# Optimization experiments

Hardware: AMD Instinct MI355X
Metric: run time of the kernel (lower is better)

## Reference

```python
import jax, jax.numpy as jnp
import numpy as np

V = 16000   # src/trg vocab
E = 512     # embedding dim (encoder_dim = decoder_dim)
H = 512     # hidden_size
L = 2       # n_layers
S = 128     # src len
T = 128     # trg len
B = 64      # batch


def _lstm_stack(x, Wih, Whh, bih, bhh, h0, c0):
    """Multi-layer LSTM, PyTorch gate order (i, f, g, o).
    x: [T, B, E]; Wih/Whh: [L, 4H, *]; bih/bhh: [L, 4H]; h0/c0: [L, B, H].
    Returns (outputs [T,B,H], hN [L,B,H], cN [L,B,H]). Dropout is eval-mode (identity)."""
    inp = x
    hs, cs = [], []
    for l in range(Wih.shape[0]):
        W1, W2 = Wih[l], Whh[l]
        b = bih[l] + bhh[l]
        def step(carry, xt, W1=W1, W2=W2, b=b):
            h, c = carry
            g = xt @ W1.T + h @ W2.T + b          # [B, 4H]
            i, f, gg, o = jnp.split(g, 4, axis=-1)
            c = jax.nn.sigmoid(f) * c + jax.nn.sigmoid(i) * jnp.tanh(gg)
            h = jax.nn.sigmoid(o) * jnp.tanh(c)
            return (h, c), h
        (h, c), ys = jax.lax.scan(step, (h0[l], c0[l]), inp)
        inp = ys
        hs.append(h)
        cs.append(c)
    return inp, jnp.stack(hs), jnp.stack(cs)


def setup_inputs() -> dict:
    key = jax.random.key(0)
    ks = jax.random.split(key, 16)
    u = lambda k, shape: jax.random.uniform(k, shape, jnp.float32, -0.08, 0.08)
    inp = {
        "src": jax.random.randint(ks[0], (S, B), 0, V),
        "trg": jax.random.randint(ks[1], (T, B), 0, V),
        "teacher_forcing_ratio": 1,
        "enc_emb": u(ks[2], (V, E)),
        "dec_emb": u(ks[3], (V, E)),
        "enc_Wih": jnp.stack([u(ks[4], (4 * H, E)), u(ks[5], (4 * H, H))]),
        "enc_Whh": u(ks[6], (L, 4 * H, H)),
        "enc_bih": u(ks[7], (L, 4 * H)),
        "enc_bhh": u(ks[8], (L, 4 * H)),
        "dec_Wih": jnp.stack([u(ks[9], (4 * H, E)), u(ks[10], (4 * H, H))]),
        "dec_Whh": u(ks[11], (L, 4 * H, H)),
        "dec_bih": u(ks[12], (L, 4 * H)),
        "dec_bhh": u(ks[13], (L, 4 * H)),
        "out_W": u(ks[14], (V, H)),
        "out_b": u(ks[15], (V,)),
    }
    return inp


def reference(src, trg, teacher_forcing_ratio, enc_emb, dec_emb,
              enc_Wih, enc_Whh, enc_bih, enc_bhh,
              dec_Wih, dec_Whh, dec_bih, dec_bhh, out_W, out_b):
    # Encoder: embed + 2-layer LSTM over src; keep final (h, c).
    zeros = jnp.zeros((L, B, H), enc_emb.dtype)
    _, h, c = _lstm_stack(enc_emb[src], enc_Wih, enc_Whh, enc_bih, enc_bhh, zeros, zeros)
    # Decoder: teacher_forcing_ratio=1 => input at step t is trg[t-1];
    # the per-step python loop collapses to one LSTM scan over trg[:-1].
    dec_in = dec_emb[trg[:-1]]                    # [T-1, B, E]
    ys, _, _ = _lstm_stack(dec_in, dec_Wih, dec_Whh, dec_bih, dec_bhh, h, c)
    logits = jnp.einsum('tbh,vh->tbv', ys, out_W) + out_b   # [T-1, B, V]
    # original: outputs[1:].view(-1, V)
    return logits.reshape(-1, V)
```

## Files before the change

kernel.cpp:

```cpp
#include <hip/hip_runtime.h>


typedef __attribute__((ext_vector_type(8))) short v8s;
typedef __attribute__((ext_vector_type(4))) short v4s;
typedef __attribute__((ext_vector_type(8))) _Float16 v8h;
typedef __attribute__((ext_vector_type(4))) float v4f;
typedef __attribute__((ext_vector_type(4))) unsigned int v4u;

#define AS1 __attribute__((address_space(1)))
#define AS3 __attribute__((address_space(3)))

__device__ __forceinline__ short f2h(float x) {
  _Float16 h = (_Float16)x;
  return __builtin_bit_cast(short, h);
}
__device__ __forceinline__ void gload16(const void* g, void* l) {
  __builtin_amdgcn_global_load_lds((const AS1 void*)g, (AS3 void*)l, 16, 0, 0);
}
__device__ __forceinline__ float sigf(float x) { return 1.f / (1.f + __expf(-x)); }
__device__ __forceinline__ float tanhfast(float x) { return 2.f / (1.f + __expf(-2.f * x)) - 1.f; }

__device__ __forceinline__ void ld16_sc1(v4u& d, const void* p) {
  asm volatile("global_load_dwordx4 %0, %1, off sc1" : "=v"(d) : "v"(p) : "memory");
}
__device__ __forceinline__ void ld16(v4u& d, const void* p) {
  asm volatile("global_load_dwordx4 %0, %1, off" : "=v"(d) : "v"(p));
}

__device__ __forceinline__ void poll32(const unsigned* flags, int base, unsigned tgt) {
  int lane = threadIdx.x & 63;
  const unsigned* fp = flags + base + (lane & 31);
  while (true) {
    unsigned v;
    asm volatile("global_load_dword %0, %1, off sc1\n\ts_waitcnt vmcnt(0)"
                 : "=v"(v) : "v"(fp) : "memory");
    if (__all((int)((lane >= 32) || (v >= tgt)))) break;
    __builtin_amdgcn_s_sleep(1);
  }
}

struct ConvJobs {
  const float* src[8];
  short* dst[8];
  int coloff[8];
};
__global__ void conv8(ConvJobs J) {
  int j = blockIdx.y;
  int i = blockIdx.x * 256 + threadIdx.x;
  int r = i >> 7, k4 = (i & 127) * 4;
  int rr = ((r >> 4) & 31) * 64 + (r >> 9) * 16 + (r & 15);
  float4 v = *(const float4*)(J.src[j] + (size_t)r * 512 + k4);
  v4s s; s[0] = f2h(v.x); s[1] = f2h(v.y); s[2] = f2h(v.z); s[3] = f2h(v.w);
  *(v4s*)(J.dst[j] + (size_t)rr * 1024 + J.coloff[j] + k4) = s;
}

__global__ void conv_ow(const float* __restrict__ in, short* __restrict__ out) {
  int i = blockIdx.x * 256 + threadIdx.x;
  if (i >= 16000 * 128) return;
  int r = i >> 7, k4 = (i & 127) * 4;
  float4 v = *(const float4*)(in + (size_t)r * 512 + k4);
  v4s s; s[0] = f2h(v.x); s[1] = f2h(v.y); s[2] = f2h(v.z); s[3] = f2h(v.w);
  *(v4s*)(out + (size_t)r * 512 + k4) = s;
}

struct BiasJobs {
  const float* a[4];
  const float* b[4];
  float* o[4];
};
__global__ void conv_b4(BiasJobs J) {
  int j = blockIdx.y;
  int r = blockIdx.x * 256 + threadIdx.x;
  if (r < 2048)
    J.o[j][((r >> 4) & 31) * 64 + (r >> 9) * 16 + (r & 15)] = J.a[j][r] + J.b[j][r];
}

__global__ void zero3(short* a, short* b, short* c, unsigned* f) {
  int i = blockIdx.x * 256 + threadIdx.x;
  if (i < 32768) { a[i] = 0; b[i] = 0; c[i] = 0; }
  if (i < 64) f[i] = 0;
}

__global__ void embed_all(const int* __restrict__ src, const int* __restrict__ trg,
                          const float* __restrict__ ee, const float* __restrict__ de,
                          short* __restrict__ out) {
  int row = blockIdx.x;
  int e = threadIdx.x * 2;
  const float* emb;
  int id;
  if (row < 8192) { id = src[row]; emb = ee; }
  else { id = trg[row - 8192]; emb = de; }
  float2 v = *(const float2*)(emb + (size_t)id * 512 + e);
  unsigned pack = ((unsigned)(unsigned short)f2h(v.y) << 16) | (unsigned short)f2h(v.x);
  *(unsigned*)(out + (size_t)row * 512 + e) = pack;
}

#define GF_BIAS 2
#define GF_GUARDM 4

__global__ __launch_bounds__(256, 2) void gemm_bt(
    const short* __restrict__ Am, const short* __restrict__ Bm,
    const float* __restrict__ bias, float* __restrict__ Cm,
    int M, int N, int K, int ldc, int flags) {
  __shared__ __align__(16) char smem[65536];
  short* lA = (short*)smem;
  short* lB = (short*)(smem + 32768);
  const int tid = threadIdx.x, lane = tid & 63, wave = tid >> 6;
  const int wm = wave >> 1, wn = wave & 1;
  const int tm = blockIdx.y, tn = blockIdx.x;
  v4f acc[4][4] = {};
  const short* Abase = Am + (size_t)tm * 128 * K;
  const short* Bbase = Bm + (size_t)tn * 128 * K;

  for (int kt = 0; kt < K; kt += 128) {
    __syncthreads();
#pragma unroll
    for (int i2 = 0; i2 < 8; ++i2) {
      int c = (wave * 8 + i2) * 64 + lane;
      int row = c >> 4, ch = c & 15;
      int sch = ch ^ (row & 15);
      gload16(Abase + (size_t)row * K + kt + sch * 8, (char*)lA + c * 16);
      gload16(Bbase + (size_t)row * K + kt + sch * 8, (char*)lB + c * 16);
    }
    asm volatile("s_waitcnt vmcnt(0)" ::: "memory");
    __syncthreads();
#pragma unroll
    for (int kc = 0; kc < 4; ++kc) {
      v8h af[4], bh[4];
#pragma unroll
      for (int mt = 0; mt < 4; ++mt) {
        int row = wm * 64 + mt * 16 + (lane & 15);
        af[mt] = *(const v8h*)((const char*)lA + row * 256 +
                               ((kc * 64 + (lane >> 4) * 16) ^ ((row & 15) << 4)));
      }
#pragma unroll
      for (int nt = 0; nt < 4; ++nt) {
        int row = wn * 64 + nt * 16 + (lane & 15);
        bh[nt] = *(const v8h*)((const char*)lB + row * 256 +
                               ((kc * 64 + (lane >> 4) * 16) ^ ((row & 15) << 4)));
      }
#pragma unroll
      for (int mt = 0; mt < 4; ++mt)
#pragma unroll
        for (int nt = 0; nt < 4; ++nt)
          acc[mt][nt] = __builtin_amdgcn_mfma_f32_16x16x32_f16(af[mt], bh[nt], acc[mt][nt], 0, 0, 0);
    }
  }

  __syncthreads();
  float* ft = (float*)smem;
#pragma unroll
  for (int mt = 0; mt < 4; ++mt)
#pragma unroll
    for (int nt = 0; nt < 4; ++nt)
#pragma unroll
      for (int rg = 0; rg < 4; ++rg) {
        int r = wm * 64 + mt * 16 + (lane >> 4) * 4 + rg;
        int c = wn * 64 + nt * 16 + (lane & 15);
        ft[r * 128 + c] = acc[mt][nt][rg];
      }
  __syncthreads();
  const int c4 = (tid & 31) * 4;
  const int gcol = tn * 128 + c4;
  float4 bv = make_float4(0.f, 0.f, 0.f, 0.f);
  if (flags & GF_BIAS) bv = *(const float4*)(bias + gcol);
#pragma unroll
  for (int it = 0; it < 16; ++it) {
    int r = it * 8 + (tid >> 5);
    int gr = tm * 128 + r;
    if ((flags & GF_GUARDM) && gr >= M) continue;
    float4 v = *(const float4*)(ft + r * 128 + c4);
    v.x += bv.x; v.y += bv.y; v.z += bv.z; v.w += bv.w;
    *(float4*)(Cm + (size_t)gr * ldc + gcol) = v;
  }
}

struct PipeArgs {
  const short* W0e;
  const short* W0d;
  const short* W1e;
  const short* W1d;
  const short* X;
  const float* b0e;
  const float* b0d;
  const float* b1e;
  const float* b1d;
  short* h0;
  short* h1;
  unsigned* flags;
  int Tenc, Ttot;
};

#define SLOT 32768

__global__ __launch_bounds__(256, 1) void lstm_pipe(PipeArgs A) {
  __shared__ __align__(16) short Wlds[64 * 1024];
  __shared__ __align__(16) short hsm[64 * 16];
  const int tid = threadIdx.x, lane = tid & 63, wave = tid >> 6;
  const int w = blockIdx.x, layer = w >> 5, wl = w & 31;

  auto stage = [&](const short* Wsrc) {
    for (int i = tid * 8; i < 64 * 1024; i += 256 * 8) {
      int row = i >> 10, k = i & 1023;
      v8s v = *(const v8s*)(Wsrc + (size_t)row * 1024 + k);
      *(v8s*)((char*)Wlds + row * 2048 + ((k * 2) ^ ((row & 7) << 4))) = v;
    }
  };
  stage((layer ? A.W1e : A.W0e) + (size_t)(wl * 64) * 1024);

  const int uu = lane & 15;
  float beV[4], bdV[4];
#pragma unroll
  for (int g = 0; g < 4; ++g) {
    beV[g] = (layer ? A.b1e : A.b0e)[wl * 64 + g * 16 + uu];
    bdV[g] = (layer ? A.b1d : A.b0d)[wl * 64 + g * 16 + uu];
  }
  float creg[4] = {0.f, 0.f, 0.f, 0.f};

  const int arow = wave * 16 + uu;
  const int koff = (lane >> 4) * 8;
  const size_t aoff = (size_t)arow * 512 + koff;
  __syncthreads();

  for (int t = 0; t < A.Ttot; ++t) {
    if (t == A.Tenc) {
      stage((layer ? A.W1d : A.W0d) + (size_t)(wl * 64) * 1024);
      __syncthreads();
    }

    v4f acc[4] = {};

    if (layer) {
      if (wave == 0) poll32(A.flags, 0, (unsigned)(t + 1));
      __syncthreads();
    }
    {
      const short* p1 = (layer ? (A.h0 + (size_t)(t + 1) * SLOT)
                               : (A.X + (size_t)t * SLOT)) + aoff;
      v4u fa[16];
      if (layer) {
#pragma unroll
        for (int kc = 0; kc < 16; ++kc) ld16_sc1(fa[kc], p1 + kc * 32);
      } else {
#pragma unroll
        for (int kc = 0; kc < 16; ++kc) ld16(fa[kc], p1 + kc * 32);
      }
      asm volatile("s_waitcnt vmcnt(0)" ::: "memory");
      __builtin_amdgcn_sched_barrier(0);
#pragma unroll
      for (int kc = 0; kc < 16; ++kc) {
        v8h af = __builtin_bit_cast(v8h, fa[kc]);
        int kg = kc * 32 + koff;
#pragma unroll
        for (int nt = 0; nt < 4; ++nt) {
          int wrow = nt * 16 + uu;
          v8h bh = *(const v8h*)((const char*)Wlds + wrow * 2048 +
                                 ((kg * 2) ^ ((wrow & 7) << 4)));
          acc[nt] = __builtin_amdgcn_mfma_f32_16x16x32_f16(af, bh, acc[nt], 0, 0, 0);
        }
      }
    }

    if (t > 0) {
      if (wave == 0) poll32(A.flags, layer ? 32 : 0, (unsigned)t);
      __syncthreads();
    }
    {
      const short* p2 = ((layer ? A.h1 : A.h0) + (size_t)t * SLOT) + aoff;
      v4u fb[16];
#pragma unroll
      for (int kc = 0; kc < 16; ++kc) ld16_sc1(fb[kc], p2 + kc * 32);
      asm volatile("s_waitcnt vmcnt(0)" ::: "memory");
      __builtin_amdgcn_sched_barrier(0);
#pragma unroll
      for (int kc = 0; kc < 16; ++kc) {
        v8h af = __builtin_bit_cast(v8h, fb[kc]);
        int kg = (kc + 16) * 32 + koff;
#pragma unroll
        for (int nt = 0; nt < 4; ++nt) {
          int wrow = nt * 16 + uu;
          v8h bh = *(const v8h*)((const char*)Wlds + wrow * 2048 +
                                 ((kg * 2) ^ ((wrow & 7) << 4)));
          acc[nt] = __builtin_amdgcn_mfma_f32_16x16x32_f16(af, bh, acc[nt], 0, 0, 0);
        }
      }
    }

    {
      const bool enc = t < A.Tenc;
      const float b0v = enc ? beV[0] : bdV[0];
      const float b1v = enc ? beV[1] : bdV[1];
      const float b2v = enc ? beV[2] : bdV[2];
      const float b3v = enc ? beV[3] : bdV[3];
#pragma unroll
      for (int rg = 0; rg < 4; ++rg) {
        float g0 = acc[0][rg] + b0v;
        float g1 = acc[1][rg] + b1v;
        float g2 = acc[2][rg] + b2v;
        float g3 = acc[3][rg] + b3v;
        float c = sigf(g1) * creg[rg] + sigf(g0) * tanhfast(g2);
        creg[rg] = c;
        float h = sigf(g3) * tanhfast(c);
        int bb = wave * 16 + ((lane >> 4) << 2) + rg;
        hsm[bb * 16 + uu] = f2h(h);
      }
    }
    __syncthreads();

    if (tid < 128) {
      int b = tid >> 1, half = tid & 1;
      v4u d = *(const v4u*)(&hsm[b * 16 + half * 8]);
      short* dst = (layer ? A.h1 : A.h0) + (size_t)(t + 1) * SLOT
                   + b * 512 + wl * 16 + half * 8;
      asm volatile("global_store_dwordx4 %0, %1, off sc1" :: "v"(dst), "v"(d) : "memory");
    }
    asm volatile("s_waitcnt vmcnt(0)" ::: "memory");
    __syncthreads();
    if (tid == 0) {
      unsigned val = (unsigned)(t + 1);
      const unsigned* fp = A.flags + w;
      asm volatile("global_store_dword %0, %1, off sc1" :: "v"(fp), "v"(val) : "memory");
    }
  }
}

extern "C" void kernel_launch(void* const* d_in, const int* in_sizes, int n_in,
                              void* d_out, int out_size, void* d_ws, size_t ws_size,
                              hipStream_t stream) {
  (void)in_sizes; (void)n_in; (void)out_size;
  const int* src = (const int*)d_in[0];
  const int* trg = (const int*)d_in[1];
  const float* enc_emb = (const float*)d_in[3];
  const float* dec_emb = (const float*)d_in[4];
  const float* enc_Wih = (const float*)d_in[5];
  const float* enc_Whh = (const float*)d_in[6];
  const float* enc_bih = (const float*)d_in[7];
  const float* enc_bhh = (const float*)d_in[8];
  const float* dec_Wih = (const float*)d_in[9];
  const float* dec_Whh = (const float*)d_in[10];
  const float* dec_bih = (const float*)d_in[11];
  const float* dec_bhh = (const float*)d_in[12];
  const float* out_W = (const float*)d_in[13];
  const float* out_b = (const float*)d_in[14];

  char* p = (char*)d_ws;
  auto alloc = [&](size_t sz) { char* r = p; p += (sz + 255) & ~(size_t)255; return r; };
  short* H0 = (short*)alloc((size_t)256 * SLOT * 2);
  short* H1 = (short*)alloc((size_t)257 * SLOT * 2);
  short* W0e = (short*)alloc((size_t)2048 * 1024 * 2);
  short* W0d = (short*)alloc((size_t)2048 * 1024 * 2);
  short* W1e = (short*)alloc((size_t)2048 * 1024 * 2);
  short* W1d = (short*)alloc((size_t)2048 * 1024 * 2);
  short* XO = (short*)alloc((size_t)255 * SLOT * 2);
  float* bE0 = (float*)alloc(2048 * 4);
  float* bE1 = (float*)alloc(2048 * 4);
  float* bD0 = (float*)alloc(2048 * 4);
  float* bD1 = (float*)alloc(2048 * 4);
  unsigned* flags = (unsigned*)alloc(256);
  size_t common = (size_t)(p - (char*)d_ws);
  const size_t owBytes = (size_t)16000 * 512 * 2;
  bool sepOW = (ws_size == 0) || (ws_size >= common + owBytes + 65536);
  short* outWb = sepOW ? (short*)alloc(owBytes) : XO;

  zero3<<<128, 256, 0, stream>>>(H0, H1, H1 + (size_t)256 * SLOT, flags);
  ConvJobs cj;
  cj.src[0] = enc_Wih;                       cj.dst[0] = W0e; cj.coloff[0] = 0;
  cj.src[1] = enc_Whh;                       cj.dst[1] = W0e; cj.coloff[1] = 512;
  cj.src[2] = dec_Wih;                       cj.dst[2] = W0d; cj.coloff[2] = 0;
  cj.src[3] = dec_Whh;                       cj.dst[3] = W0d; cj.coloff[3] = 512;
  cj.src[4] = enc_Wih + (size_t)2048 * 512;  cj.dst[4] = W1e; cj.coloff[4] = 0;
  cj.src[5] = enc_Whh + (size_t)2048 * 512;  cj.dst[5] = W1e; cj.coloff[5] = 512;
  cj.src[6] = dec_Wih + (size_t)2048 * 512;  cj.dst[6] = W1d; cj.coloff[6] = 0;
  cj.src[7] = dec_Whh + (size_t)2048 * 512;  cj.dst[7] = W1d; cj.coloff[7] = 512;
  conv8<<<dim3(1024, 8), 256, 0, stream>>>(cj);
  BiasJobs bj;
  bj.a[0] = enc_bih;        bj.b[0] = enc_bhh;        bj.o[0] = bE0;
  bj.a[1] = enc_bih + 2048; bj.b[1] = enc_bhh + 2048; bj.o[1] = bE1;
  bj.a[2] = dec_bih;        bj.b[2] = dec_bhh;        bj.o[2] = bD0;
  bj.a[3] = dec_bih + 2048; bj.b[3] = dec_bhh + 2048; bj.o[3] = bD1;
  conv_b4<<<dim3(8, 4), 256, 0, stream>>>(bj);
  embed_all<<<16320, 256, 0, stream>>>(src, trg, enc_emb, dec_emb, XO);
  if (sepOW) conv_ow<<<8000, 256, 0, stream>>>(out_W, outWb);

  PipeArgs pa = {W0e, W0d, W1e, W1d, XO, bE0, bD0, bE1, bD1,
                 H0, H1, flags, 128, 255};
  lstm_pipe<<<64, 256, 0, stream>>>(pa);

  if (!sepOW) conv_ow<<<8000, 256, 0, stream>>>(out_W, outWb);

  gemm_bt<<<dim3(125, 64), 256, 0, stream>>>(H1 + (size_t)129 * SLOT, outWb, out_b,
                                             (float*)d_out, 8128, 16000, 512, 16000,
                                             GF_BIAS | GF_GUARDM);
}
```

Before: 2.261 ms.

## Overlap output projection GEMM with decoder LSTM via persistent worker blocks

Fuses the LSTM pipeline and the vocabulary projection GEMM into one kernel launch. 192 extra blocks pull GEMM tiles from an atomic work queue and poll layer-1 progress flags, so each 128-row output tile is computed as soon as its decoder timesteps are done. This hides most of the large GEMM behind the latency-bound recurrent loop. It risks slowing the LSTM blocks through contention for CUs and memory bandwidth, and it relies on all 256 blocks being co-resident to avoid deadlock.

```diff
diff --git a/kernel.cpp b/kernel.cpp
--- a/kernel.cpp
+++ b/kernel.cpp
@@ -36,6 +36,17 @@
                  : "=v"(v) : "v"(fp) : "memory");
     if (__all((int)((lane >= 32) || (v >= tgt)))) break;
     __builtin_amdgcn_s_sleep(1);
+  }
+}
+__device__ __forceinline__ void poll_l1(const unsigned* flags, unsigned thr) {
+  int lane = threadIdx.x & 63;
+  const unsigned* fp = flags + 32 + (lane & 31);
+  while (true) {
+    unsigned v;
+    asm volatile("global_load_dword %0, %1, off sc1\n\ts_waitcnt vmcnt(0)"
+                 : "=v"(v) : "v"(fp) : "memory");
+    if (__all((int)((lane >= 32) || (v >= thr)))) break;
+    __builtin_amdgcn_s_sleep(64);
   }
 }
 
@@ -78,7 +89,7 @@
 __global__ void zero3(short* a, short* b, short* c, unsigned* f) {
   int i = blockIdx.x * 256 + threadIdx.x;
   if (i < 32768) { a[i] = 0; b[i] = 0; c[i] = 0; }
-  if (i < 64) f[i] = 0;
+  if (i < 128) f[i] = 0;
 }
 
 __global__ void embed_all(const int* __restrict__ src, const int* __restrict__ trg,
@@ -97,17 +108,15 @@
 
 #define GF_BIAS 2
 #define GF_GUARDM 4
-
-__global__ __launch_bounds__(256, 2) void gemm_bt(
-    const short* __restrict__ Am, const short* __restrict__ Bm,
-    const float* __restrict__ bias, float* __restrict__ Cm,
-    int M, int N, int K, int ldc, int flags) {
-  __shared__ __align__(16) char smem[65536];
+#define SLOT 32768
+
+__device__ __forceinline__ void gemm_tile128(
+    const short* Am, const short* Bm, const float* bias, float* Cm,
+    int M, int K, int ldc, int tm, int tn, int flags, char* smem) {
   short* lA = (short*)smem;
   short* lB = (short*)(smem + 32768);
   const int tid = threadIdx.x, lane = tid & 63, wave = tid >> 6;
   const int wm = wave >> 1, wn = wave & 1;
-  const int tm = blockIdx.y, tn = blockIdx.x;
   v4f acc[4][4] = {};
   const short* Abase = Am + (size_t)tm * 128 * K;
   const short* Bbase = Bm + (size_t)tn * 128 * K;
@@ -175,7 +184,15 @@
   }
 }
 
-struct PipeArgs {
+__global__ __launch_bounds__(256, 2) void gemm_bt(
+    const short* __restrict__ Am, const short* __restrict__ Bm,
+    const float* __restrict__ bias, float* __restrict__ Cm,
+    int M, int N, int K, int ldc, int flags) {
+  __shared__ __align__(16) char smem[65536];
+  gemm_tile128(Am, Bm, bias, Cm, M, K, ldc, blockIdx.y, blockIdx.x, flags, smem);
+}
+
+struct FusedArgs {
   const short* W0e;
   const short* W0d;
   const short* W1e;
@@ -188,16 +205,42 @@
   short* h0;
   short* h1;
   unsigned* flags;
+  const short* Bgem;
+  const float* obias;
+  float* Cout;
   int Tenc, Ttot;
+  int workers;
 };
 
-#define SLOT 32768
-
-__global__ __launch_bounds__(256, 1) void lstm_pipe(PipeArgs A) {
-  __shared__ __align__(16) short Wlds[64 * 1024];
-  __shared__ __align__(16) short hsm[64 * 16];
+__global__ __launch_bounds__(256, 1) void lstm_fused(FusedArgs A) {
+  __shared__ __align__(16) char smem[133120];
   const int tid = threadIdx.x, lane = tid & 63, wave = tid >> 6;
-  const int w = blockIdx.x, layer = w >> 5, wl = w & 31;
+  const int bid = blockIdx.x;
+
+  if (bid >= 64) {
+    int* sQ = (int*)(smem + 131072);
+    unsigned* wq = A.flags + 64;
+    while (true) {
+      if (tid == 0)
+        *sQ = (int)__hip_atomic_fetch_add(wq, 1u, __ATOMIC_RELAXED,
+                                          __HIP_MEMORY_SCOPE_AGENT);
+      __syncthreads();
+      int id = *sQ;
+      __syncthreads();
+      if (id >= 8000) break;
+      int tm = id / 125, tn = id - tm * 125;
+      unsigned thr = 130 + 2 * tm; if (thr > 255) thr = 255;
+      if (wave == 0) poll_l1(A.flags, thr);
+      __syncthreads();
+      gemm_tile128(A.h1 + (size_t)129 * SLOT, A.Bgem, A.obias, A.Cout,
+                   8128, 512, 16000, tm, tn, GF_BIAS | GF_GUARDM, smem);
+    }
+    return;
+  }
+
+  short* Wlds = (short*)smem;
+  short* hsm = (short*)(smem + 131072);
+  const int w = bid, layer = w >> 5, wl = w & 31;
 
   auto stage = [&](const short* Wsrc) {
     for (int i = tid * 8; i < 64 * 1024; i += 256 * 8) {
@@ -356,7 +399,7 @@
   float* bE1 = (float*)alloc(2048 * 4);
   float* bD0 = (float*)alloc(2048 * 4);
   float* bD1 = (float*)alloc(2048 * 4);
-  unsigned* flags = (unsigned*)alloc(256);
+  unsigned* flags = (unsigned*)alloc(512);
   size_t common = (size_t)(p - (char*)d_ws);
   const size_t owBytes = (size_t)16000 * 512 * 2;
   bool sepOW = (ws_size == 0) || (ws_size >= common + owBytes + 65536);
@@ -382,13 +425,17 @@
   embed_all<<<16320, 256, 0, stream>>>(src, trg, enc_emb, dec_emb, XO);
   if (sepOW) conv_ow<<<8000, 256, 0, stream>>>(out_W, outWb);
 
-  PipeArgs pa = {W0e, W0d, W1e, W1d, XO, bE0, bD0, bE1, bD1,
-                 H0, H1, flags, 128, 255};
-  lstm_pipe<<<64, 256, 0, stream>>>(pa);
-
-  if (!sepOW) conv_ow<<<8000, 256, 0, stream>>>(out_W, outWb);
-
-  gemm_bt<<<dim3(125, 64), 256, 0, stream>>>(H1 + (size_t)129 * SLOT, outWb, out_b,
-                                             (float*)d_out, 8128, 16000, 512, 16000,
-                                             GF_BIAS | GF_GUARDM);
-}
+  FusedArgs fa = {W0e, W0d, W1e, W1d, XO, bE0, bD0, bE1, bD1,
+                  H0, H1, flags, outWb, out_b, (float*)d_out, 128, 255,
+                  sepOW ? 192 : 0};
+
+  if (sepOW) {
+    lstm_fused<<<256, 256, 0, stream>>>(fa);
+  } else {
+    lstm_fused<<<64, 256, 0, stream>>>(fa);
+    conv_ow<<<8000, 256, 0, stream>>>(out_W, outWb);
+    gemm_bt<<<dim3(125, 64), 256, 0, stream>>>(H1 + (size_t)129 * SLOT, outWb, out_b,
+                                               (float*)d_out, 8128, 16000, 512, 16000,
+                                               GF_BIAS | GF_GUARDM);
+  }
+}
```

New measurement: 2.064 ms (median of 2 runs). -8.7%, faster.
